# Performance work log

Hardware: AMD Instinct MI355X
Metric: run time of the kernel (lower is better)

## Reference

```python
import jax, jax.numpy as jnp
import numpy as np

N_NODES = 50000
N_EDGES = 1600000
N_GRAPHS = 64
DIM_IN, DIM_H, HEADS, DIM_OUT = 128, 32, 2, 64
NEG_SLOPE = 0.2


def _segment_softmax(scores, seg, num_segments):
    # scores: [E, H], seg: [E] int -> softmax over edges sharing the same dst
    m = jax.ops.segment_max(scores, seg, num_segments=num_segments)
    m = jnp.where(jnp.isfinite(m), m, 0.0)  # empty segments -> -inf; neutralize
    e = jnp.exp(scores - m[seg])
    s = jax.ops.segment_sum(e, seg, num_segments=num_segments)
    return e / (s[seg] + 1e-16)


def gatv2_conv(x, edge_index, Wl, Wr, att, bias, heads, ch, n_nodes):
    # PyG GATv2Conv defaults: add_self_loops=True, share_weights=False, concat heads.
    loops = jnp.arange(n_nodes, dtype=edge_index.dtype)
    ei = jnp.concatenate([edge_index, jnp.stack([loops, loops])], axis=1)
    src, dst = ei[0], ei[1]
    xl = (x @ Wl).reshape(n_nodes, heads, ch)  # source transform
    xr = (x @ Wr).reshape(n_nodes, heads, ch)  # target transform
    el = xl[src]                               # [E+N, H, C] gather
    s = jax.nn.leaky_relu(el + xr[dst], NEG_SLOPE)
    scores = jnp.einsum('ehc,hc->eh', s, att)  # [E+N, H]
    alpha = _segment_softmax(scores, dst, n_nodes)
    out = jax.ops.segment_sum(alpha[..., None] * el, dst, num_segments=n_nodes)
    return out.reshape(n_nodes, heads * ch) + bias


def setup_inputs() -> dict:
    key = jax.random.key(0)
    ks = jax.random.split(key, 12)
    glorot = lambda k, shp: jax.random.normal(k, shp, jnp.float32) * np.sqrt(2.0 / (shp[0] + shp[-1]))
    x = jax.random.normal(ks[0], (N_NODES, DIM_IN), jnp.float32)
    edge_index = jax.random.randint(ks[1], (2, N_EDGES), 0, N_NODES, jnp.int64)
    batch = jnp.sort(jax.random.randint(ks[2], (N_NODES,), 0, N_GRAPHS, jnp.int64))
    H1 = DIM_H * HEADS
    return {
        'x': x, 'edge_index': edge_index, 'batch': batch,
        'Wl1': glorot(ks[3], (DIM_IN, H1)), 'Wr1': glorot(ks[4], (DIM_IN, H1)),
        'att1': glorot(ks[5], (HEADS, DIM_H)), 'b1': jnp.zeros((H1,), jnp.float32),
        'Wl2': glorot(ks[6], (H1, DIM_OUT)), 'Wr2': glorot(ks[7], (H1, DIM_OUT)),
        'att2': glorot(ks[8], (1, DIM_OUT)), 'b2': jnp.zeros((DIM_OUT,), jnp.float32),
        'lin_w': glorot(ks[9], (DIM_OUT, 2)), 'lin_b': jnp.zeros((2,), jnp.float32),
    }


def reference(x, edge_index, batch, Wl1, Wr1, att1, b1, Wl2, Wr2, att2, b2, lin_w, lin_b):
    # eval mode: dropout is identity
    h = gatv2_conv(x, edge_index, Wl1, Wr1, att1, b1, HEADS, DIM_H, N_NODES)
    h = jax.nn.elu(h)
    h = jax.nn.elu(gatv2_conv(h, edge_index, Wl2, Wr2, att2, b2, 1, DIM_OUT, N_NODES))
    # global mean pool over graphs
    sums = jax.ops.segment_sum(h, batch, num_segments=N_GRAPHS)
    cnts = jax.ops.segment_sum(jnp.ones((N_NODES,), h.dtype), batch, num_segments=N_GRAPHS)
    pooled = sums / jnp.maximum(cnts, 1.0)[:, None]
    return pooled @ lin_w + lin_b
```

## Files before the change

### kernel.cpp

```cpp
#include <hip/hip_runtime.h>
#include <hip/hip_bf16.h>
#include <math.h>

#define N_NODES 50000
#define N_EDGES 1600000
#define N_GRAPHS 64
#define NB 391
#define NBLK 256
#define CHUNK 6250
#define ROW_STRIDE 80

typedef unsigned int u32;

template <int CTRL>
__device__ __forceinline__ float dpp_add(float v) {
    int r = __builtin_amdgcn_update_dpp(0, __builtin_bit_cast(int, v), CTRL, 0xF, 0xF, true);
    return v + __builtin_bit_cast(float, r);
}

__device__ __forceinline__ float red8(float v) {
    v = dpp_add<0xB1>(v);
    v = dpp_add<0x4E>(v);
    v = dpp_add<0x141>(v);
    return v;
}

__device__ __forceinline__ float red16(float v) {
    v = red8(v);
    v = dpp_add<0x140>(v);
    return v;
}

__device__ __forceinline__ float4 lrelu4(float4 u) {
    float4 r;
    r.x = fmaxf(u.x, 0.2f * u.x);
    r.y = fmaxf(u.y, 0.2f * u.y);
    r.z = fmaxf(u.z, 0.2f * u.z);
    r.w = fmaxf(u.w, 0.2f * u.w);
    return r;
}

__device__ __forceinline__ float4 unpack_bf16x4(uint2 u) {
    float4 a;
    a.x = __builtin_bit_cast(float, u.x << 16);
    a.y = __builtin_bit_cast(float, u.x & 0xFFFF0000u);
    a.z = __builtin_bit_cast(float, u.y << 16);
    a.w = __builtin_bit_cast(float, u.y & 0xFFFF0000u);
    return a;
}

__device__ __forceinline__ u32 pack_bf16x2(float lo, float hi) {
    unsigned short l = __builtin_bit_cast(unsigned short, __float2bfloat16(lo));
    unsigned short h = __builtin_bit_cast(unsigned short, __float2bfloat16(hi));
    return (u32)l | ((u32)h << 16);
}

template <int K, bool FUSE_COUNT>
__global__ __launch_bounds__(256) void gemm_tiled(
    const float* __restrict__ x, const float* __restrict__ Wl,
    const float* __restrict__ Wr, u32* __restrict__ xlb, float* __restrict__ xr,
    const int* __restrict__ ei, int* __restrict__ countsRM, int gemmBlocks) {
    __shared__ float xs[64][K + 1];
    const int t = threadIdx.x;
    if (FUSE_COUNT && blockIdx.x >= gemmBlocks) {
        int* h = (int*)&xs[0][0];
        const int cb = blockIdx.x - gemmBlocks;
        for (int k = t; k < NB; k += 256) h[k] = 0;
        __syncthreads();
        const int base = cb * CHUNK;
        for (int e = base + t; e < base + CHUNK; e += 256)
            atomicAdd(&h[ei[N_EDGES + e] >> 7], 1);
        __syncthreads();
        for (int k = t; k < NB; k += 256) countsRM[cb * NB + k] = h[k];
        return;
    }
    const int base = blockIdx.x * 64;
    const int nf4 = 64 * K / 4;
    for (int f = t; f < nf4; f += 256) {
        const int row = f / (K / 4);
        const int c4 = f % (K / 4);
        float4 v = make_float4(0.f, 0.f, 0.f, 0.f);
        if (base + row < N_NODES)
            v = *(const float4*)(x + (size_t)(base + row) * K + c4 * 4);
        xs[row][c4 * 4 + 0] = v.x;
        xs[row][c4 * 4 + 1] = v.y;
        xs[row][c4 * 4 + 2] = v.z;
        xs[row][c4 * 4 + 3] = v.w;
    }
    __syncthreads();
    const int lane = t & 63;
    const int w = __builtin_amdgcn_readfirstlane(t >> 6);
    const float* __restrict__ W = (w < 2) ? Wl : Wr;
    const int cb = (w & 1) * 32;
    float acc[32];
#pragma unroll
    for (int j = 0; j < 32; ++j) acc[j] = 0.f;
#pragma unroll 2
    for (int k = 0; k < K; ++k) {
        const float xv = xs[lane][k];
        const float* __restrict__ Wrow = W + k * 64 + cb;
#pragma unroll
        for (int j = 0; j < 32; ++j) acc[j] = fmaf(xv, Wrow[j], acc[j]);
    }
    const int n = base + lane;
    if (n < N_NODES) {
        if (w < 2) {
            u32 pk[16];
#pragma unroll
            for (int j = 0; j < 32; j += 2) pk[j >> 1] = pack_bf16x2(acc[j], acc[j + 1]);
            uint4* dst = (uint4*)(xlb + (size_t)n * 32 + (w & 1) * 16);
#pragma unroll
            for (int j = 0; j < 4; ++j)
                dst[j] = make_uint4(pk[j * 4], pk[j * 4 + 1], pk[j * 4 + 2], pk[j * 4 + 3]);
        } else {
#pragma unroll
            for (int j = 0; j < 32; j += 4) {
                float4 v = {acc[j], acc[j + 1], acc[j + 2], acc[j + 3]};
                *(float4*)(xr + (size_t)n * 64 + cb + j) = v;
            }
        }
    }
}

__global__ __launch_bounds__(256) void scan_bucket(
    const int* __restrict__ countsRM, int* __restrict__ scanT,
    int* __restrict__ totals) {
    __shared__ int tmp[256];
    const int b = blockIdx.x;
    const int t = threadIdx.x;
    const int v0 = countsRM[t * NB + b];
    tmp[t] = v0;
    __syncthreads();
    for (int off = 1; off < 256; off <<= 1) {
        int v = (t >= off) ? tmp[t - off] : 0;
        __syncthreads();
        tmp[t] += v;
        __syncthreads();
    }
    scanT[b * 256 + t] = tmp[t] - v0;
    if (t == 255) totals[b] = tmp[t];
}

__global__ __launch_bounds__(512) void scan_total(
    const int* __restrict__ totals, int* __restrict__ bucketBase) {
    __shared__ int tmp[512];
    const int t = threadIdx.x;
    const int v0 = (t < NB) ? totals[t] : 0;
    tmp[t] = v0;
    __syncthreads();
    for (int off = 1; off < 512; off <<= 1) {
        int v = (t >= off) ? tmp[t - off] : 0;
        __syncthreads();
        tmp[t] += v;
        __syncthreads();
    }
    if (t < NB) bucketBase[t] = tmp[t] - v0;
    if (t == NB - 1) bucketBase[NB] = tmp[t];
}

__global__ __launch_bounds__(256) void scatter2_kernel(
    const int* __restrict__ ei, const int* __restrict__ scanT,
    const int* __restrict__ bucketBase, int* __restrict__ sortedE) {
    __shared__ int cursor[NB];
    const int t = threadIdx.x;
    const int b = blockIdx.x;
    for (int k = t; k < NB; k += 256)
        cursor[k] = bucketBase[k] + scanT[k * 256 + b];
    __syncthreads();
    const int base = b * CHUNK;
    for (int e = base + t; e < base + CHUNK; e += 256) {
        const int s = ei[e];
        const int d = ei[N_EDGES + e];
        const int idx = atomicAdd(&cursor[d >> 7], 1);
        sortedE[idx] = (s << 7) | (d & 127);
    }
}

__global__ __launch_bounds__(256) void expand_kernel(
    const int* __restrict__ bucketBase, const int* __restrict__ sortedE,
    int* __restrict__ deg, int* __restrict__ rows) {
    __shared__ int ldeg[128];
    const int b = blockIdx.x;
    const int t = threadIdx.x;
    if (t < 128) ldeg[t] = 0;
    __syncthreads();
    const int beg = bucketBase[b];
    const int end = bucketBase[b + 1];
    const int node_base = b * 128;
    for (int i = beg + t; i < end; i += 256) {
        const int en = sortedE[i];
        const int ld = en & 127;
        const int pos = atomicAdd(&ldeg[ld], 1);
        if (pos < ROW_STRIDE) rows[(node_base + ld) * ROW_STRIDE + pos] = en >> 7;
    }
    __syncthreads();
    if (t < 128) {
        const int n = node_base + t;
        if (n < N_NODES) {
            int c = ldeg[t];
            deg[n] = c < ROW_STRIDE ? c : ROW_STRIDE;
        }
    }
}

template <bool L1HEADS>
__device__ __forceinline__ float edge_ev4(float4 a, float4 xr4, float4 at4, bool valid) {
    float4 u;
    u.x = a.x + xr4.x; u.y = a.y + xr4.y; u.z = a.z + xr4.z; u.w = a.w + xr4.w;
    float4 l = lrelu4(u);
    float v = at4.x * l.x;
    v = fmaf(at4.y, l.y, v);
    v = fmaf(at4.z, l.z, v);
    v = fmaf(at4.w, l.w, v);
    v = L1HEADS ? red8(v) : red16(v);
    float ev = __expf(v);
    return valid ? ev : 0.f;
}

template <bool L1HEADS>
__global__ __launch_bounds__(256) void node_layer(
    const int* __restrict__ deg, const int* __restrict__ rows,
    const u32* __restrict__ xlb, const float* __restrict__ xr,
    const float* __restrict__ att, const float* __restrict__ bias,
    float* __restrict__ hout) {
    const int n = (blockIdx.x * 256 + threadIdx.x) >> 6;
    const int lane = threadIdx.x & 63;
    const int sub = lane & 15;
    const int g = lane >> 4;
    const float4 xr4 = *(const float4*)(xr + (size_t)n * 64 + sub * 4);
    const float4 xl4 = unpack_bf16x4(*(const uint2*)(xlb + (size_t)n * 32 + sub * 2));
    const float4 at4 = *(const float4*)(att + sub * 4);

    float ev = edge_ev4<L1HEADS>(xl4, xr4, at4, g == 0);
    float4 acc;
    acc.x = ev * xl4.x; acc.y = ev * xl4.y; acc.z = ev * xl4.z; acc.w = ev * xl4.w;
    float ssum = ev;

    const int cnt = __builtin_amdgcn_readfirstlane(deg[n]);
    const int* __restrict__ row = rows + n * ROW_STRIDE;
    for (int i = 0; i < cnt; i += 8) {
        const int e0 = i + g, e1 = i + 4 + g;
        const bool v0 = e0 < cnt, v1 = e1 < cnt;
        const int s0 = v0 ? row[e0] : 0;
        const int s1 = v1 ? row[e1] : 0;
        const float4 a0 = unpack_bf16x4(*(const uint2*)(xlb + (size_t)s0 * 32 + sub * 2));
        const float4 a1 = unpack_bf16x4(*(const uint2*)(xlb + (size_t)s1 * 32 + sub * 2));
        const float ev0 = edge_ev4<L1HEADS>(a0, xr4, at4, v0);
        const float ev1 = edge_ev4<L1HEADS>(a1, xr4, at4, v1);
        acc.x = fmaf(ev0, a0.x, acc.x); acc.x = fmaf(ev1, a1.x, acc.x);
        acc.y = fmaf(ev0, a0.y, acc.y); acc.y = fmaf(ev1, a1.y, acc.y);
        acc.z = fmaf(ev0, a0.z, acc.z); acc.z = fmaf(ev1, a1.z, acc.z);
        acc.w = fmaf(ev0, a0.w, acc.w); acc.w = fmaf(ev1, a1.w, acc.w);
        ssum += ev0 + ev1;
    }
    acc.x += __shfl_xor(acc.x, 16); acc.x += __shfl_xor(acc.x, 32);
    acc.y += __shfl_xor(acc.y, 16); acc.y += __shfl_xor(acc.y, 32);
    acc.z += __shfl_xor(acc.z, 16); acc.z += __shfl_xor(acc.z, 32);
    acc.w += __shfl_xor(acc.w, 16); acc.w += __shfl_xor(acc.w, 32);
    ssum  += __shfl_xor(ssum, 16);  ssum  += __shfl_xor(ssum, 32);
    if (g == 0) {
        const float inv = 1.f / (ssum + 1e-16f);
        const float4 b4 = *(const float4*)(bias + sub * 4);
        float4 o;
        o.x = acc.x * inv + b4.x;
        o.y = acc.y * inv + b4.y;
        o.z = acc.z * inv + b4.z;
        o.w = acc.w * inv + b4.w;
        o.x = o.x > 0.f ? o.x : expm1f(o.x);
        o.y = o.y > 0.f ? o.y : expm1f(o.y);
        o.z = o.z > 0.f ? o.z : expm1f(o.z);
        o.w = o.w > 0.f ? o.w : expm1f(o.w);
        *(float4*)(hout + (size_t)n * 64 + sub * 4) = o;
    }
}

__global__ __launch_bounds__(64) void pool_kernel(
    const float* __restrict__ h2, const int* __restrict__ batch,
    float* __restrict__ pooled, float* __restrict__ cnt) {
    const int t = threadIdx.x;
    const int base = blockIdx.x * 64;
    float local = 0.f, lc = 0.f;
    int cur = -1;
    for (int j = 0; j < 64; ++j) {
        const int n = base + j;
        if (n >= N_NODES) break;
        const int g = batch[n];
        if (g != cur) {
            if (cur >= 0) {
                unsafeAtomicAdd(&pooled[cur * 64 + t], local);
                if (t == 0) unsafeAtomicAdd(&cnt[cur], lc);
            }
            cur = g; local = 0.f; lc = 0.f;
        }
        local += h2[n * 64 + t];
        lc += 1.f;
    }
    if (cur >= 0) {
        unsafeAtomicAdd(&pooled[cur * 64 + t], local);
        if (t == 0) unsafeAtomicAdd(&cnt[cur], lc);
    }
}

__global__ __launch_bounds__(128) void head_kernel(
    const float* __restrict__ pooled, const float* __restrict__ cnt,
    const float* __restrict__ lin_w, const float* __restrict__ lin_b,
    float* __restrict__ out) {
    const int i = threadIdx.x;
    const int g = i >> 1, k = i & 1;
    float c = cnt[g];
    c = c > 1.f ? c : 1.f;
    float a = 0.f;
#pragma unroll
    for (int j = 0; j < 64; ++j) a = fmaf(pooled[g * 64 + j] / c, lin_w[j * 2 + k], a);
    out[i] = a + lin_b[k];
}

extern "C" void kernel_launch(void* const* d_in, const int* in_sizes, int n_in,
                              void* d_out, int out_size, void* d_ws, size_t ws_size,
                              hipStream_t stream) {
    const float* x     = (const float*)d_in[0];
    const int*   ei    = (const int*)d_in[1];
    const int*   batch = (const int*)d_in[2];
    const float* Wl1   = (const float*)d_in[3];
    const float* Wr1   = (const float*)d_in[4];
    const float* att1  = (const float*)d_in[5];
    const float* b1    = (const float*)d_in[6];
    const float* Wl2   = (const float*)d_in[7];
    const float* Wr2   = (const float*)d_in[8];
    const float* att2  = (const float*)d_in[9];
    const float* b2    = (const float*)d_in[10];
    const float* lin_w = (const float*)d_in[11];
    const float* lin_b = (const float*)d_in[12];

    float* ws = (float*)d_ws;
    u32*   xlb      = (u32*)ws;
    float* xr       = ws + 1600000;
    float* h1       = ws + 4800000;
    int*   rows     = (int*)(ws + 8000000);
    int*   deg      = (int*)(ws + 12003840);
    int*   countsRM = (int*)(ws + 12053888);
    int*   scanT    = (int*)(ws + 12153984);
    int*   totals   = (int*)(ws + 12254080);
    int*   bb       = (int*)(ws + 12254592);
    float* pooled   = ws + 12255104;
    float* cnt      = ws + 12259200;
    int*   sortedE  = (int*)(ws + 12259264);

    hipMemsetAsync(pooled, 0, (size_t)(4096 + 64) * sizeof(float), stream);

    const int gblocks = (N_NODES + 63) / 64;

    gemm_tiled<128, true><<<gblocks + NBLK, 256, 0, stream>>>(
        x, Wl1, Wr1, xlb, xr, ei, countsRM, gblocks);

    scan_bucket<<<NB, 256, 0, stream>>>(countsRM, scanT, totals);
    scan_total<<<1, 512, 0, stream>>>(totals, bb);
    scatter2_kernel<<<NBLK, 256, 0, stream>>>(ei, scanT, bb, sortedE);
    expand_kernel<<<NB, 256, 0, stream>>>(bb, sortedE, deg, rows);

    node_layer<true><<<N_NODES / 4, 256, 0, stream>>>(deg, rows, xlb, xr, att1, b1, h1);

    gemm_tiled<64, false><<<gblocks, 256, 0, stream>>>(
        h1, Wl2, Wr2, xlb, xr, nullptr, nullptr, gblocks);
    node_layer<false><<<N_NODES / 4, 256, 0, stream>>>(deg, rows, xlb, xr, att2, b2, h1);

    pool_kernel<<<(N_NODES + 63) / 64, 64, 0, stream>>>(h1, batch, pooled, cnt);
    head_kernel<<<1, 128, 0, stream>>>(pooled, cnt, lin_w, lin_b, (float*)d_out);
}
```

Before: 318.9 us.

## Split leaky-ReLU into linear plus abs terms and widen per-lane edge vectors

Rewrites leaky_relu(u) as 0.6u+0.4|u| so that the linear part of the attention score, att·xl[src] and att·xr[dst], is precomputed per node in the GEMM epilogue. The edge loop then needs only the abs term. The node kernel now processes 8 edges per iteration with 8 lanes each reading 8 bf16 channels as one uint4. Self-loops are stored in the adjacency rows, and each row is padded to a multiple of 8 with a sentinel node whose alpha is -1e30, which removes the per-edge validity branches. The cost is extra per-node alpha arrays, sentinel writes in expand, and fewer cross-lane reduction steps traded for more shuffles at the end.

```diff
diff --git a/kernel.cpp b/kernel.cpp
--- a/kernel.cpp
+++ b/kernel.cpp
@@ -9,8 +9,11 @@
 #define NBLK 256
 #define CHUNK 6250
 #define ROW_STRIDE 80
+#define SENT 50047
 
 typedef unsigned int u32;
+
+__device__ __forceinline__ float bcf(u32 u) { return __builtin_bit_cast(float, u); }
 
 template <int CTRL>
 __device__ __forceinline__ float dpp_add(float v) {
@@ -18,37 +21,6 @@
     return v + __builtin_bit_cast(float, r);
 }
 
-__device__ __forceinline__ float red8(float v) {
-    v = dpp_add<0xB1>(v);
-    v = dpp_add<0x4E>(v);
-    v = dpp_add<0x141>(v);
-    return v;
-}
-
-__device__ __forceinline__ float red16(float v) {
-    v = red8(v);
-    v = dpp_add<0x140>(v);
-    return v;
-}
-
-__device__ __forceinline__ float4 lrelu4(float4 u) {
-    float4 r;
-    r.x = fmaxf(u.x, 0.2f * u.x);
-    r.y = fmaxf(u.y, 0.2f * u.y);
-    r.z = fmaxf(u.z, 0.2f * u.z);
-    r.w = fmaxf(u.w, 0.2f * u.w);
-    return r;
-}
-
-__device__ __forceinline__ float4 unpack_bf16x4(uint2 u) {
-    float4 a;
-    a.x = __builtin_bit_cast(float, u.x << 16);
-    a.y = __builtin_bit_cast(float, u.x & 0xFFFF0000u);
-    a.z = __builtin_bit_cast(float, u.y << 16);
-    a.w = __builtin_bit_cast(float, u.y & 0xFFFF0000u);
-    return a;
-}
-
 __device__ __forceinline__ u32 pack_bf16x2(float lo, float hi) {
     unsigned short l = __builtin_bit_cast(unsigned short, __float2bfloat16(lo));
     unsigned short h = __builtin_bit_cast(unsigned short, __float2bfloat16(hi));
@@ -58,7 +30,9 @@
 template <int K, bool FUSE_COUNT>
 __global__ __launch_bounds__(256) void gemm_tiled(
     const float* __restrict__ x, const float* __restrict__ Wl,
-    const float* __restrict__ Wr, u32* __restrict__ xlb, float* __restrict__ xr,
+    const float* __restrict__ Wr, const float* __restrict__ att,
+    u32* __restrict__ xlb, float* __restrict__ xr,
+    float* __restrict__ alb, float* __restrict__ arb,
     const int* __restrict__ ei, int* __restrict__ countsRM, int gemmBlocks) {
     __shared__ float xs[64][K + 1];
     const int t = threadIdx.x;
@@ -104,7 +78,11 @@
     }
     const int n = base + lane;
     if (n < N_NODES) {
+        float av = 0.f;
+#pragma unroll
+        for (int j = 0; j < 32; ++j) av = fmaf(att[cb + j], acc[j], av);
         if (w < 2) {
+            alb[(size_t)n * 2 + (w & 1)] = av;
             u32 pk[16];
 #pragma unroll
             for (int j = 0; j < 32; j += 2) pk[j >> 1] = pack_bf16x2(acc[j], acc[j + 1]);
@@ -113,6 +91,7 @@
             for (int j = 0; j < 4; ++j)
                 dst[j] = make_uint4(pk[j * 4], pk[j * 4 + 1], pk[j * 4 + 2], pk[j * 4 + 3]);
         } else {
+            arb[(size_t)n * 2 + (w & 1)] = av;
 #pragma unroll
             for (int j = 0; j < 32; j += 4) {
                 float4 v = {acc[j], acc[j + 1], acc[j + 2], acc[j + 3]};
@@ -142,7 +121,8 @@
 }
 
 __global__ __launch_bounds__(512) void scan_total(
-    const int* __restrict__ totals, int* __restrict__ bucketBase) {
+    const int* __restrict__ totals, int* __restrict__ bucketBase,
+    float* __restrict__ alb) {
     __shared__ int tmp[512];
     const int t = threadIdx.x;
     const int v0 = (t < NB) ? totals[t] : 0;
@@ -156,6 +136,7 @@
     }
     if (t < NB) bucketBase[t] = tmp[t] - v0;
     if (t == NB - 1) bucketBase[NB] = tmp[t];
+    if (t == 0) { alb[(size_t)SENT * 2] = -1e30f; alb[(size_t)SENT * 2 + 1] = -1e30f; }
 }
 
 __global__ __launch_bounds__(256) void scatter2_kernel(
@@ -182,95 +163,102 @@
     __shared__ int ldeg[128];
     const int b = blockIdx.x;
     const int t = threadIdx.x;
-    if (t < 128) ldeg[t] = 0;
+    const int node_base = b * 128;
+    if (t < 128) {
+        const int n = node_base + t;
+        ldeg[t] = 1;
+        if (n < N_NODES) rows[(size_t)n * ROW_STRIDE] = n;
+    }
     __syncthreads();
     const int beg = bucketBase[b];
     const int end = bucketBase[b + 1];
-    const int node_base = b * 128;
     for (int i = beg + t; i < end; i += 256) {
         const int en = sortedE[i];
         const int ld = en & 127;
         const int pos = atomicAdd(&ldeg[ld], 1);
-        if (pos < ROW_STRIDE) rows[(node_base + ld) * ROW_STRIDE + pos] = en >> 7;
+        if (pos < ROW_STRIDE) rows[(size_t)(node_base + ld) * ROW_STRIDE + pos] = en >> 7;
     }
     __syncthreads();
     if (t < 128) {
         const int n = node_base + t;
         if (n < N_NODES) {
             int c = ldeg[t];
-            deg[n] = c < ROW_STRIDE ? c : ROW_STRIDE;
+            c = c < ROW_STRIDE ? c : ROW_STRIDE;
+            const int cp = (c + 7) & ~7;
+            for (int j = c; j < cp; ++j) rows[(size_t)n * ROW_STRIDE + j] = SENT;
+            deg[n] = cp;
         }
     }
 }
 
-template <bool L1HEADS>
-__device__ __forceinline__ float edge_ev4(float4 a, float4 xr4, float4 at4, bool valid) {
-    float4 u;
-    u.x = a.x + xr4.x; u.y = a.y + xr4.y; u.z = a.z + xr4.z; u.w = a.w + xr4.w;
-    float4 l = lrelu4(u);
-    float v = at4.x * l.x;
-    v = fmaf(at4.y, l.y, v);
-    v = fmaf(at4.z, l.z, v);
-    v = fmaf(at4.w, l.w, v);
-    v = L1HEADS ? red8(v) : red16(v);
-    float ev = __expf(v);
-    return valid ? ev : 0.f;
-}
-
-template <bool L1HEADS>
+template <bool L1>
 __global__ __launch_bounds__(256) void node_layer(
     const int* __restrict__ deg, const int* __restrict__ rows,
     const u32* __restrict__ xlb, const float* __restrict__ xr,
+    const float* __restrict__ alb, const float* __restrict__ arb,
     const float* __restrict__ att, const float* __restrict__ bias,
     float* __restrict__ hout) {
     const int n = (blockIdx.x * 256 + threadIdx.x) >> 6;
     const int lane = threadIdx.x & 63;
-    const int sub = lane & 15;
-    const int g = lane >> 4;
-    const float4 xr4 = *(const float4*)(xr + (size_t)n * 64 + sub * 4);
-    const float4 xl4 = unpack_bf16x4(*(const uint2*)(xlb + (size_t)n * 32 + sub * 2));
-    const float4 at4 = *(const float4*)(att + sub * 4);
-
-    float ev = edge_ev4<L1HEADS>(xl4, xr4, at4, g == 0);
-    float4 acc;
-    acc.x = ev * xl4.x; acc.y = ev * xl4.y; acc.z = ev * xl4.z; acc.w = ev * xl4.w;
-    float ssum = ev;
-
-    const int cnt = __builtin_amdgcn_readfirstlane(deg[n]);
-    const int* __restrict__ row = rows + n * ROW_STRIDE;
-    for (int i = 0; i < cnt; i += 8) {
-        const int e0 = i + g, e1 = i + 4 + g;
-        const bool v0 = e0 < cnt, v1 = e1 < cnt;
-        const int s0 = v0 ? row[e0] : 0;
-        const int s1 = v1 ? row[e1] : 0;
-        const float4 a0 = unpack_bf16x4(*(const uint2*)(xlb + (size_t)s0 * 32 + sub * 2));
-        const float4 a1 = unpack_bf16x4(*(const uint2*)(xlb + (size_t)s1 * 32 + sub * 2));
-        const float ev0 = edge_ev4<L1HEADS>(a0, xr4, at4, v0);
-        const float ev1 = edge_ev4<L1HEADS>(a1, xr4, at4, v1);
-        acc.x = fmaf(ev0, a0.x, acc.x); acc.x = fmaf(ev1, a1.x, acc.x);
-        acc.y = fmaf(ev0, a0.y, acc.y); acc.y = fmaf(ev1, a1.y, acc.y);
-        acc.z = fmaf(ev0, a0.z, acc.z); acc.z = fmaf(ev1, a1.z, acc.z);
-        acc.w = fmaf(ev0, a0.w, acc.w); acc.w = fmaf(ev1, a1.w, acc.w);
-        ssum += ev0 + ev1;
-    }
-    acc.x += __shfl_xor(acc.x, 16); acc.x += __shfl_xor(acc.x, 32);
-    acc.y += __shfl_xor(acc.y, 16); acc.y += __shfl_xor(acc.y, 32);
-    acc.z += __shfl_xor(acc.z, 16); acc.z += __shfl_xor(acc.z, 32);
-    acc.w += __shfl_xor(acc.w, 16); acc.w += __shfl_xor(acc.w, 32);
-    ssum  += __shfl_xor(ssum, 16);  ssum  += __shfl_xor(ssum, 32);
+    const int sub = lane & 7;
+    const int g = lane >> 3;
+    const float4 xra = *(const float4*)(xr + (size_t)n * 64 + sub * 8);
+    const float4 xrb = *(const float4*)(xr + (size_t)n * 64 + sub * 8 + 4);
+    const float4 ata = *(const float4*)(att + sub * 8);
+    const float4 atb = *(const float4*)(att + sub * 8 + 4);
+    const float2 ar2 = *(const float2*)(arb + (size_t)n * 2);
+    const float based = 0.6f * (L1 ? ((sub & 4) ? ar2.y : ar2.x) : (ar2.x + ar2.y));
+
+    float c0 = 0.f, c1 = 0.f, c2 = 0.f, c3 = 0.f;
+    float c4 = 0.f, c5 = 0.f, c6 = 0.f, c7 = 0.f;
+    float ssum = 0.f;
+    const int cp = __builtin_amdgcn_readfirstlane(deg[n]);
+    const int* __restrict__ row = rows + (size_t)n * ROW_STRIDE;
+    for (int i = 0; i < cp; i += 8) {
+        const int s = row[i + g];
+        float als;
+        if (L1) {
+            als = alb[(size_t)s * 2 + ((sub >> 2) & 1)];
+        } else {
+            const float2 a2 = *(const float2*)(alb + (size_t)s * 2);
+            als = a2.x + a2.y;
+        }
+        const uint4 r4 = *(const uint4*)(xlb + (size_t)s * 32 + sub * 4);
+        const float a0 = bcf(r4.x << 16), a1 = bcf(r4.x & 0xFFFF0000u);
+        const float a2f = bcf(r4.y << 16), a3 = bcf(r4.y & 0xFFFF0000u);
+        const float a4 = bcf(r4.z << 16), a5 = bcf(r4.z & 0xFFFF0000u);
+        const float a6 = bcf(r4.w << 16), a7 = bcf(r4.w & 0xFFFF0000u);
+        float v = ata.x * fabsf(a0 + xra.x);
+        v = fmaf(ata.y, fabsf(a1 + xra.y), v);
+        v = fmaf(ata.z, fabsf(a2f + xra.z), v);
+        v = fmaf(ata.w, fabsf(a3 + xra.w), v);
+        v = fmaf(atb.x, fabsf(a4 + xrb.x), v);
+        v = fmaf(atb.y, fabsf(a5 + xrb.y), v);
+        v = fmaf(atb.z, fabsf(a6 + xrb.z), v);
+        v = fmaf(atb.w, fabsf(a7 + xrb.w), v);
+        v = dpp_add<0xB1>(v);
+        v = dpp_add<0x4E>(v);
+        if (!L1) v = dpp_add<0x141>(v);
+        const float ev = __expf(fmaf(0.6f, als, fmaf(0.4f, v, based)));
+        c0 = fmaf(ev, a0, c0); c1 = fmaf(ev, a1, c1);
+        c2 = fmaf(ev, a2f, c2); c3 = fmaf(ev, a3, c3);
+        c4 = fmaf(ev, a4, c4); c5 = fmaf(ev, a5, c5);
+        c6 = fmaf(ev, a6, c6); c7 = fmaf(ev, a7, c7);
+        ssum += ev;
+    }
+#define XRED(x) x += __shfl_xor(x, 8); x += __shfl_xor(x, 16); x += __shfl_xor(x, 32);
+    XRED(c0) XRED(c1) XRED(c2) XRED(c3) XRED(c4) XRED(c5) XRED(c6) XRED(c7) XRED(ssum)
+#undef XRED
     if (g == 0) {
         const float inv = 1.f / (ssum + 1e-16f);
-        const float4 b4 = *(const float4*)(bias + sub * 4);
-        float4 o;
-        o.x = acc.x * inv + b4.x;
-        o.y = acc.y * inv + b4.y;
-        o.z = acc.z * inv + b4.z;
-        o.w = acc.w * inv + b4.w;
-        o.x = o.x > 0.f ? o.x : expm1f(o.x);
-        o.y = o.y > 0.f ? o.y : expm1f(o.y);
-        o.z = o.z > 0.f ? o.z : expm1f(o.z);
-        o.w = o.w > 0.f ? o.w : expm1f(o.w);
-        *(float4*)(hout + (size_t)n * 64 + sub * 4) = o;
+        const float4 ba = *(const float4*)(bias + sub * 8);
+        const float4 bb = *(const float4*)(bias + sub * 8 + 4);
+        float o[8] = {c0 * inv + ba.x, c1 * inv + ba.y, c2 * inv + ba.z, c3 * inv + ba.w,
+                      c4 * inv + bb.x, c5 * inv + bb.y, c6 * inv + bb.z, c7 * inv + bb.w};
+#pragma unroll
+        for (int j = 0; j < 8; ++j) o[j] = o[j] > 0.f ? o[j] : expm1f(o[j]);
+        *(float4*)(hout + (size_t)n * 64 + sub * 8) = make_float4(o[0], o[1], o[2], o[3]);
+        *(float4*)(hout + (size_t)n * 64 + sub * 8 + 4) = make_float4(o[4], o[5], o[6], o[7]);
     }
 }
 
@@ -334,35 +322,39 @@
 
     float* ws = (float*)d_ws;
     u32*   xlb      = (u32*)ws;
-    float* xr       = ws + 1600000;
-    float* h1       = ws + 4800000;
-    int*   rows     = (int*)(ws + 8000000);
-    int*   deg      = (int*)(ws + 12003840);
-    int*   countsRM = (int*)(ws + 12053888);
-    int*   scanT    = (int*)(ws + 12153984);
-    int*   totals   = (int*)(ws + 12254080);
-    int*   bb       = (int*)(ws + 12254592);
-    float* pooled   = ws + 12255104;
-    float* cnt      = ws + 12259200;
-    int*   sortedE  = (int*)(ws + 12259264);
+    float* xr       = ws + 1601536;
+    float* h1       = ws + 4801536;
+    float* alb      = ws + 8001536;
+    float* arb      = ws + 8101632;
+    int*   rows     = (int*)(ws + 8201728);
+    int*   deg      = (int*)(ws + 12205568);
+    int*   countsRM = (int*)(ws + 12255616);
+    int*   scanT    = (int*)(ws + 12355712);
+    int*   totals   = (int*)(ws + 12455808);
+    int*   bb       = (int*)(ws + 12456320);
+    float* pooled   = ws + 12456832;
+    float* cnt      = ws + 12460928;
+    int*   sortedE  = (int*)(ws + 12460992);
 
     hipMemsetAsync(pooled, 0, (size_t)(4096 + 64) * sizeof(float), stream);
 
     const int gblocks = (N_NODES + 63) / 64;
 
     gemm_tiled<128, true><<<gblocks + NBLK, 256, 0, stream>>>(
-        x, Wl1, Wr1, xlb, xr, ei, countsRM, gblocks);
+        x, Wl1, Wr1, att1, xlb, xr, alb, arb, ei, countsRM, gblocks);
 
     scan_bucket<<<NB, 256, 0, stream>>>(countsRM, scanT, totals);
-    scan_total<<<1, 512, 0, stream>>>(totals, bb);
+    scan_total<<<1, 512, 0, stream>>>(totals, bb, alb);
     scatter2_kernel<<<NBLK, 256, 0, stream>>>(ei, scanT, bb, sortedE);
     expand_kernel<<<NB, 256, 0, stream>>>(bb, sortedE, deg, rows);
 
-    node_layer<true><<<N_NODES / 4, 256, 0, stream>>>(deg, rows, xlb, xr, att1, b1, h1);
+    node_layer<true><<<N_NODES / 4, 256, 0, stream>>>(
+        deg, rows, xlb, xr, alb, arb, att1, b1, h1);
 
     gemm_tiled<64, false><<<gblocks, 256, 0, stream>>>(
-        h1, Wl2, Wr2, xlb, xr, nullptr, nullptr, gblocks);
-    node_layer<false><<<N_NODES / 4, 256, 0, stream>>>(deg, rows, xlb, xr, att2, b2, h1);
+        h1, Wl2, Wr2, att2, xlb, xr, alb, arb, nullptr, nullptr, gblocks);
+    node_layer<false><<<N_NODES / 4, 256, 0, stream>>>(
+        deg, rows, xlb, xr, alb, arb, att2, b2, h1);
 
     pool_kernel<<<(N_NODES + 63) / 64, 64, 0, stream>>>(h1, batch, pooled, cnt);
     head_kernel<<<1, 128, 0, stream>>>(pooled, cnt, lin_w, lin_b, (float*)d_out);
```

Measured after the change: 311.4 us. -2.3%, faster.
